# Kernel optimization log

Measured on AMD Instinct MI355X. Metric: run time of the kernel, lower is better.

The kernel has to match this reference:

```python
import jax, jax.numpy as jnp
import numpy as np
import math

H = 32          # num heads
D_NOPE = 128
D_ROPE = 64
D_QK = D_NOPE + D_ROPE   # 192
D_V = 128
KV_LORA = 512
EPS = 1e-6
ROPE_THETA = 10000.0
FACTOR = 40.0
BETA_FAST, BETA_SLOW = 32.0, 1.0
ORIG_MAX_POS = 4096
MSCALE_ALL_DIM = 1.0


def _yarn_inv_freq():
    dim = D_ROPE
    pos_freqs = ROPE_THETA ** (np.arange(0, dim, 2, dtype=np.float64) / dim)
    inv_extra = 1.0 / pos_freqs
    inv_inter = 1.0 / (FACTOR * pos_freqs)

    def corr_dim(n_rot):
        return dim * math.log(ORIG_MAX_POS / (n_rot * 2 * math.pi)) / (2 * math.log(ROPE_THETA))
    low = max(math.floor(corr_dim(BETA_FAST)), 0)
    high = min(math.ceil(corr_dim(BETA_SLOW)), dim - 1)
    ramp = np.clip((np.arange(dim // 2, dtype=np.float64) - low) / max(high - low, 1e-3), 0, 1)
    inv_freq_mask = 1.0 - ramp  # extrapolation_factor = 1
    inv_freq = inv_inter * (1 - inv_freq_mask) + inv_extra * inv_freq_mask
    return jnp.asarray(inv_freq, dtype=jnp.float32)  # [D_ROPE//2]


def _apply_rope_gptj(x, cos, sin):
    # x: [T, n, D_ROPE]; cos/sin: [T, D_ROPE//2]; interleaved (is_neox_style=False)
    x2 = x.reshape(*x.shape[:-1], D_ROPE // 2, 2)
    x1, xo = x2[..., 0], x2[..., 1]
    c = cos[:, None, :]
    s = sin[:, None, :]
    r1 = x1 * c - xo * s
    r2 = xo * c + x1 * s
    return jnp.stack([r1, r2], axis=-1).reshape(x.shape)


def _rmsnorm(x, w):
    var = jnp.mean(x.astype(jnp.float32) ** 2, axis=-1, keepdims=True)
    return (x * jax.lax.rsqrt(var + EPS)) * w


def setup_inputs() -> dict:
    key = jax.random.key(0)
    ks = jax.random.split(key, 8)
    T, HID = 2048, 4096
    def w(k, shape, fan_in):
        return jax.random.normal(k, shape, dtype=jnp.float32) * (1.0 / math.sqrt(fan_in))
    return {
        "positions": jnp.arange(T, dtype=jnp.int32),
        "hidden_states": jax.random.normal(ks[0], (T, HID), dtype=jnp.float32),
        "Wqa": w(ks[1], (HID, 1536), HID),
        "q_a_ln": jnp.ones((1536,), dtype=jnp.float32),
        "Wqb": w(ks[2], (1536, H * D_QK), 1536),
        "Wkva": w(ks[3], (HID, KV_LORA + D_ROPE), HID),
        "kv_a_ln": jnp.ones((KV_LORA,), dtype=jnp.float32),
        "Wkvb": w(ks[4], (KV_LORA, H * (D_NOPE + D_V)), KV_LORA),
        "Wo": w(ks[5], (H * D_V, HID), H * D_V),
    }


def reference(positions, hidden_states, Wqa, q_a_ln, Wqb, Wkva, kv_a_ln, Wkvb, Wo):
    T = hidden_states.shape[0]
    # softmax scaling with yarn mscale correction
    mscale = 0.1 * MSCALE_ALL_DIM * math.log(FACTOR) + 1.0
    scaling = (D_QK ** -0.5) * mscale * mscale

    # --- low-rank Q path ---
    q = hidden_states @ Wqa                       # [T, 1536]
    q = _rmsnorm(q, q_a_ln)
    q = (q @ Wqb).reshape(T, H, D_QK)             # [T, H, 192]
    q_nope, q_pe = q[..., :D_NOPE], q[..., D_NOPE:]

    # --- low-rank latent KV path ---
    latent = hidden_states @ Wkva                 # [T, 576]
    kv_a = _rmsnorm(latent[:, :KV_LORA], kv_a_ln) # [T, 512]
    k_pe = latent[:, None, KV_LORA:]              # [T, 1, 64]
    kv = (kv_a @ Wkvb).reshape(T, H, D_NOPE + D_V)
    k_nope = kv[..., :D_NOPE]                     # [T, H, 128]
    v = kv[..., D_NOPE:]                          # [T, H, 128]

    # --- decoupled RoPE on rope slice only ---
    inv_freq = _yarn_inv_freq()
    freqs = positions.astype(jnp.float32)[:, None] * inv_freq[None, :]  # [T, 32]
    cos, sin = jnp.cos(freqs), jnp.sin(freqs)
    q_pe = _apply_rope_gptj(q_pe, cos, sin)       # [T, H, 64]
    k_pe = _apply_rope_gptj(k_pe, cos, sin)       # [T, 1, 64]

    q = jnp.concatenate([q_nope, q_pe], axis=-1)                      # [T, H, 192]
    k = jnp.concatenate([k_nope, jnp.broadcast_to(k_pe, (T, H, D_ROPE))], axis=-1)

    # --- causal MHA over assembled K/V ---
    scores = jnp.einsum('thd,shd->hts', q, k) * scaling               # [H, T, T]
    causal = positions[None, :, None] >= positions[None, None, :]
    scores = jnp.where(causal, scores, jnp.finfo(scores.dtype).min)
    probs = jax.nn.softmax(scores, axis=-1)
    attn = jnp.einsum('hts,shd->thd', probs, v).reshape(T, H * D_V)
    return attn @ Wo                                                   # [T, 4096]
```

## Files before the change

kernel.cpp:

```cpp
#include <hip/hip_runtime.h>
#include <math.h>

typedef __bf16 bf16x8 __attribute__((ext_vector_type(8)));
typedef float f32x4 __attribute__((ext_vector_type(4)));
typedef unsigned short u16;
typedef unsigned int u32;

#define T_SEQ 2048
#define NHEAD 32

__device__ __forceinline__ u16 f2bu(float f){
  u32 u = __float_as_uint(f);
  u32 r = (u + 0x7fffu + ((u >> 16) & 1u)) >> 16;
  return (u16)r;
}

__device__ __forceinline__ void gload_lds16(const void* g, void* l){
  __builtin_amdgcn_global_load_lds((const __attribute__((address_space(1))) u32*)g,
                                   (__attribute__((address_space(3))) u32*)l, 16, 0, 0);
}

__global__ void cast_f32_bf16(const float* __restrict__ in, u16* __restrict__ out, int n4){
  int i = blockIdx.x * blockDim.x + threadIdx.x;
  int stride = gridDim.x * blockDim.x;
  for (; i < n4; i += stride){
    float4 v = ((const float4*)in)[i];
    ushort4 o;
    o.x = f2bu(v.x); o.y = f2bu(v.y); o.z = f2bu(v.z); o.w = f2bu(v.w);
    ((ushort4*)out)[i] = o;
  }
}

__device__ __forceinline__ void tc_body(const float* __restrict__ src, u16* __restrict__ dst,
                                        int K, int N, int k0, int n0){
  __shared__ float tile[64][65];
  int t = threadIdx.x;
  int rr = t >> 4, c4 = (t & 15) * 4;
  #pragma unroll
  for (int i = 0; i < 4; i++){
    int r = rr + i * 16;
    int n = n0 + c4;
    float4 v;
    if (n < N) v = *(const float4*)(src + (size_t)(k0 + r) * N + n);
    else       v = make_float4(0.f, 0.f, 0.f, 0.f);
    tile[r][c4]     = v.x;
    tile[r][c4 + 1] = v.y;
    tile[r][c4 + 2] = v.z;
    tile[r][c4 + 3] = v.w;
  }
  __syncthreads();
  #pragma unroll
  for (int i = 0; i < 4; i++){
    int n = rr + i * 16;
    ushort4 o;
    o.x = f2bu(tile[c4 + 0][n]);
    o.y = f2bu(tile[c4 + 1][n]);
    o.z = f2bu(tile[c4 + 2][n]);
    o.w = f2bu(tile[c4 + 3][n]);
    *(ushort4*)(dst + (size_t)(n0 + n) * K + k0 + c4) = o;
  }
}

__global__ __launch_bounds__(256) void transpose_batch(
    const float* __restrict__ Wqa, u16* __restrict__ WqaT,
    const float* __restrict__ Wkva, u16* __restrict__ WkvaT,
    const float* __restrict__ Wqb, u16* __restrict__ WqbT,
    const float* __restrict__ Wkvb, u16* __restrict__ WkvbT,
    const float* __restrict__ Wo, u16* __restrict__ WoT){
  int bid = blockIdx.x;
  const float* s; u16* d; int K, N, gx, l;
  if (bid < 1536)      { s = Wqa;  d = WqaT;  K = 4096; N = 1536; gx = 64; l = bid; }
  else if (bid < 2176) { s = Wkva; d = WkvaT; K = 4096; N = 576;  gx = 64; l = bid - 1536; }
  else if (bid < 4480) { s = Wqb;  d = WqbT;  K = 1536; N = 6144; gx = 24; l = bid - 2176; }
  else if (bid < 5504) { s = Wkvb; d = WkvbT; K = 512;  N = 8192; gx = 8;  l = bid - 4480; }
  else                 { s = Wo;   d = WoT;   K = 4096; N = 4096; gx = 64; l = bid - 5504; }
  tc_body(s, d, K, N, (l % gx) * 64, (l / gx) * 64);
}

__global__ void rope_table(const int* __restrict__ positions, float* __restrict__ cosT,
                           float* __restrict__ sinT, float lo, float denom){
  int idx = blockIdx.x * blockDim.x + threadIdx.x;
  if (idx >= T_SEQ * 32) return;
  int t = idx >> 5, i = idx & 31;
  float pf = powf(10000.f, (float)i / 32.f);
  float inv_extra = 1.f / pf;
  float inv_inter = 1.f / (40.f * pf);
  float ramp = fminf(fmaxf(((float)i - lo) / denom, 0.f), 1.f);
  float invf = inv_inter * ramp + inv_extra * (1.f - ramp);
  float fr = (float)positions[t] * invf;
  cosT[idx] = cosf(fr);
  sinT[idx] = sinf(fr);
}

__global__ void rmsnorm_cast(const float* __restrict__ in, int istride, int n,
                             const float* __restrict__ w, u16* __restrict__ out, int ostride){
  int row = blockIdx.x;
  const float* x = in + (size_t)row * istride;
  float ss = 0.f;
  for (int c = threadIdx.x; c < n; c += blockDim.x){ float v = x[c]; ss += v * v; }
  #pragma unroll
  for (int off = 1; off < 64; off <<= 1) ss += __shfl_xor(ss, off);
  __shared__ float wsum[4];
  if ((threadIdx.x & 63) == 0) wsum[threadIdx.x >> 6] = ss;
  __syncthreads();
  float tot = wsum[0] + wsum[1] + wsum[2] + wsum[3];
  float scale = rsqrtf(tot / (float)n + 1e-6f);
  for (int c = threadIdx.x; c < n; c += blockDim.x)
    out[(size_t)row * ostride + c] = f2bu(x[c] * scale * w[c]);
}

__global__ void rope_kpe(const float* __restrict__ lat, int lstride, int loff,
                         const float* __restrict__ cosT,
                         const float* __restrict__ sinT, u16* __restrict__ kpe){
  int idx = blockIdx.x * blockDim.x + threadIdx.x;
  if (idx >= T_SEQ * 32) return;
  int t = idx >> 5, i = idx & 31;
  float x1 = lat[(size_t)t * lstride + loff + 2 * i];
  float x2 = lat[(size_t)t * lstride + loff + 2 * i + 1];
  float c = cosT[idx], s = sinT[idx];
  kpe[t * 64 + 2 * i]     = f2bu(x1 * c - x2 * s);
  kpe[t * 64 + 2 * i + 1] = f2bu(x2 * c + x1 * s);
}

__global__ void build_vt(const u16* __restrict__ Vtmp, u16* __restrict__ Vt){
  __shared__ u16 tile[128][72];
  int t0 = blockIdx.x * 64;
  int h = blockIdx.y;
  #pragma unroll
  for (int i = 0; i < 32; i++){
    int lin = threadIdx.x + i * 256;
    int tt = lin >> 7, dd = lin & 127;
    tile[dd][tt] = Vtmp[(size_t)(t0 + tt) * 4096 + h * 128 + dd];
  }
  __syncthreads();
  #pragma unroll
  for (int i = 0; i < 32; i++){
    int lin = threadIdx.x + i * 256;
    int dd = lin >> 6, tt = lin & 63;
    Vt[(size_t)(h * 128 + dd) * T_SEQ + t0 + tt] = tile[dd][tt];
  }
}

template<int EPI>
__global__ __launch_bounds__(256) void gemm_bt(const u16* __restrict__ A, const u16* __restrict__ BT,
                                               float* __restrict__ C, u16* __restrict__ O1,
                                               u16* __restrict__ O2,
                                               const float* __restrict__ cosT,
                                               const float* __restrict__ sinT,
                                               float scaling, int M, int N, int K){
  __shared__ __align__(1024) char lds[32768];
  const int tid = threadIdx.x;
  const int wave = tid >> 6, lane = tid & 63;
  const int lg = lane >> 4, lm = lane & 15;

  int gx = gridDim.x;
  int nwg = gx * gridDim.y;
  int orig = blockIdx.y * gx + blockIdx.x;
  int qq = nwg >> 3, rr_ = nwg & 7, xc = orig & 7, rest = orig >> 3;
  int wg = (xc < rr_ ? xc * (qq + 1) : rr_ * (qq + 1) + (xc - rr_) * qq) + rest;
  const int bn = (wg % gx) * 128, bm = (wg / gx) * 128;

  const int wr = (wave >> 1) * 64, wc = (wave & 1) * 64;
  f32x4 acc[4][4] = {};
  int srow[2], scol[2], soff[2];
  #pragma unroll
  for (int j = 0; j < 2; j++){
    int o = (wave * 2 + j) * 1024 + lane * 16;
    int row = o >> 6;
    int cg = ((o >> 4) & 3) ^ ((row >> 1) & 3);
    srow[j] = row; scol[j] = cg * 8; soff[j] = (wave * 2 + j) * 1024;
  }

  #pragma unroll
  for (int j = 0; j < 2; j++){
    gload_lds16(A  + (size_t)(bm + srow[j]) * K + scol[j], lds + soff[j]);
    gload_lds16(BT + (size_t)(bn + srow[j]) * K + scol[j], lds + 16384 + soff[j]);
  }

  int cur = 0;
  for (int k0 = 0; k0 < K; k0 += 32){
    if (k0 + 32 < K){
      char* dA = lds + (cur ^ 1) * 8192;
      char* dB = lds + 16384 + (cur ^ 1) * 8192;
      #pragma unroll
      for (int j = 0; j < 2; j++){
        gload_lds16(A  + (size_t)(bm + srow[j]) * K + k0 + 32 + scol[j], dA + soff[j]);
        gload_lds16(BT + (size_t)(bn + srow[j]) * K + k0 + 32 + scol[j], dB + soff[j]);
      }
      asm volatile("s_waitcnt vmcnt(4)" ::: "memory");
    } else {
      asm volatile("s_waitcnt vmcnt(0)" ::: "memory");
    }
    __builtin_amdgcn_sched_barrier(0);
    __builtin_amdgcn_s_barrier();

    const char* ldsA = lds + cur * 8192;
    const char* ldsB = lds + 16384 + cur * 8192;
    bf16x8 af[4], bfr[4];
    #pragma unroll
    for (int m = 0; m < 4; m++){
      int r = wr + m * 16 + lm;
      af[m] = *(const bf16x8*)(ldsA + r * 64 + ((lg ^ ((r >> 1) & 3)) << 4));
    }
    #pragma unroll
    for (int n = 0; n < 4; n++){
      int r = wc + n * 16 + lm;
      bfr[n] = *(const bf16x8*)(ldsB + r * 64 + ((lg ^ ((r >> 1) & 3)) << 4));
    }
    __builtin_amdgcn_s_setprio(1);
    #pragma unroll
    for (int m = 0; m < 4; m++)
      #pragma unroll
      for (int n = 0; n < 4; n++)
        acc[m][n] = __builtin_amdgcn_mfma_f32_16x16x32_bf16(af[m], bfr[n], acc[m][n], 0, 0, 0);
    __builtin_amdgcn_s_setprio(0);
    __builtin_amdgcn_s_barrier();
    cur ^= 1;
  }

  #pragma unroll
  for (int m = 0; m < 4; m++)
    #pragma unroll
    for (int n = 0; n < 4; n++)
      #pragma unroll
      for (int q = 0; q < 4; q++){
        int r = bm + wr + m * 16 + lg * 4 + q;
        int c = bn + wc + n * 16 + lm;
        float v = acc[m][n][q];
        if (EPI == 0){
          C[(size_t)r * N + c] = v;
        } else if (EPI == 1){
          float vp = __shfl_xor(v, 1);
          int h = c / 192, d = c - h * 192;
          float outv;
          if (d < 128) outv = v;
          else {
            int i = (d - 128) >> 1;
            float co = cosT[r * 32 + i], si = sinT[r * 32 + i];
            outv = (d & 1) ? (v * co + vp * si) : (v * co - vp * si);
          }
          O1[(size_t)h * T_SEQ * 192 + (size_t)r * 192 + d] = f2bu(outv * scaling);
        } else {
          int h = c >> 8, d = c & 255;
          if (d < 128) O1[(size_t)h * T_SEQ * 128 + (size_t)r * 128 + d] = f2bu(v);
          else         O2[(size_t)r * 4096 + h * 128 + (d - 128)] = f2bu(v);
        }
      }
}

__global__ __launch_bounds__(512, 4) void flash_attn(const u16* __restrict__ Qp, const u16* __restrict__ Kp,
                                                     const u16* __restrict__ kpe, const u16* __restrict__ Vt,
                                                     u16* __restrict__ attnb){
  const int b = blockIdx.x;
  const int h = (b & 7) + 8 * ((b >> 3) & 3);
  const int qt = 15 - (b >> 5);
  const int tid = threadIdx.x;
  const int wave = tid >> 6, lane = tid & 63;
  const int lg = lane >> 4, lm = lane & 15;
  const int qbase = qt * 128 + wave * 16;

  __shared__ __align__(1024) char lds[51200];
  u16* Pw = (u16*)(lds + 40960 + wave * 1280);

  const u16* KpH = Kp + (size_t)h * T_SEQ * 128;
  const u16* VtH = Vt + (size_t)h * 128 * T_SEQ;

  int kO[2], kLoc[2], kPE[2];
  #pragma unroll
  for (int j = 0; j < 2; j++){
    int o = tid + 512 * j;
    int r = (o / 24) & 31, c = o % 24;
    int cx = c ^ (r & 7);
    kO[j] = o * 16;
    if (cx < 16){ kPE[j] = 0; kLoc[j] = r * 128 + cx * 8; }
    else        { kPE[j] = 1; kLoc[j] = r * 64 + (cx - 16) * 8; }
  }
  int vO, vSrc;
  { int o = tid; int d = o >> 2, c = o & 3; vO = o * 16; vSrc = d * T_SEQ + ((c ^ ((d >> 1) & 3)) << 3); }

  #define STAGE_KV(t, bi)                                                              \
    do {                                                                               \
      char* _k = lds + (bi) * 12288;                                                   \
      char* _v = lds + 24576 + (bi) * 8192;                                            \
      { const u16* _s = kPE[0] ? (kpe + (size_t)(t) * 2048 + kLoc[0])                  \
                               : (KpH + (size_t)(t) * 4096 + kLoc[0]);                 \
        gload_lds16(_s, _k + kO[0]); }                                                 \
      if (tid < 256){                                                                  \
        const u16* _s = kPE[1] ? (kpe + (size_t)(t) * 2048 + kLoc[1])                  \
                               : (KpH + (size_t)(t) * 4096 + kLoc[1]);                 \
        gload_lds16(_s, _k + kO[1]); }                                                 \
      gload_lds16(VtH + vSrc + (t) * 32, _v + vO);                                     \
    } while (0)

  const int nt = 4 * qt + 4;

  bf16x8 qf[6];
  const u16* Qbase = Qp + (size_t)(h * T_SEQ + qbase + lm) * 192 + lg * 8;
  #pragma unroll
  for (int dk = 0; dk < 6; dk++) qf[dk] = *(const bf16x8*)(Qbase + dk * 32);

  f32x4 o_[8] = {};
  float m_[4], l_[4];
  #pragma unroll
  for (int q = 0; q < 4; q++){ m_[q] = -3.0e38f; l_[q] = 0.f; }

  STAGE_KV(0, 0);

  #pragma unroll 1
  for (int kt = 0; kt < nt; kt++){
    const int t0 = kt * 32;
    const int bsel = kt & 1;
    asm volatile("s_waitcnt vmcnt(0)" ::: "memory");
    __builtin_amdgcn_sched_barrier(0);
    __builtin_amdgcn_s_barrier();
    if (kt + 1 < nt) STAGE_KV(kt + 1, bsel ^ 1);
    const char* Kb = lds + bsel * 12288;
    const char* Vb = lds + 24576 + bsel * 8192;

    f32x4 s_[2] = {};
    __builtin_amdgcn_s_setprio(1);
    #pragma unroll
    for (int hh = 0; hh < 2; hh++){
      const int r = hh * 16 + lm;
      const int rb = r * 384, rx = r & 7;
      #pragma unroll
      for (int dk = 0; dk < 6; dk++){
        bf16x8 kf = *(const bf16x8*)(Kb + rb + (((dk * 4 + lg) ^ rx) << 4));
        s_[hh] = __builtin_amdgcn_mfma_f32_16x16x32_bf16(qf[dk], kf, s_[hh], 0, 0, 0);
      }
    }
    __builtin_amdgcn_s_setprio(0);
    #pragma unroll
    for (int hh = 0; hh < 2; hh++)
      #pragma unroll
      for (int q = 0; q < 4; q++){
        int col = t0 + hh * 16 + lm;
        int qrow = qbase + lg * 4 + q;
        if (col > qrow) s_[hh][q] = -3.0e38f;
      }
    float pm[4];
    #pragma unroll
    for (int q = 0; q < 4; q++) pm[q] = fmaxf(s_[0][q], s_[1][q]);
    int ok = (pm[0] <= m_[0] + 8.f) & (pm[1] <= m_[1] + 8.f) &
             (pm[2] <= m_[2] + 8.f) & (pm[3] <= m_[3] + 8.f);
    if (!__all(ok)){
      #pragma unroll
      for (int q = 0; q < 4; q++){
        float v = pm[q];
        #pragma unroll
        for (int off = 8; off; off >>= 1) v = fmaxf(v, __shfl_xor(v, off));
        float mn = fmaxf(m_[q], v);
        float alpha = (m_[q] <= -1.0e37f) ? 0.f : exp2f(m_[q] - mn);
        l_[q] *= alpha;
        #pragma unroll
        for (int n = 0; n < 8; n++) o_[n][q] *= alpha;
        m_[q] = mn;
      }
    }
    #pragma unroll
    for (int q = 0; q < 4; q++){
      #pragma unroll
      for (int hh = 0; hh < 2; hh++){
        float p = exp2f(s_[hh][q] - m_[q]);
        l_[q] += p;
        Pw[(lg * 4 + q) * 40 + hh * 16 + lm] = f2bu(p);
      }
    }
    asm volatile("s_waitcnt lgkmcnt(0)" ::: "memory");
    __builtin_amdgcn_sched_barrier(0);
    bf16x8 pf = *(const bf16x8*)((const char*)Pw + lm * 80 + lg * 16);
    __builtin_amdgcn_s_setprio(1);
    #pragma unroll
    for (int n = 0; n < 8; n++){
      const int d = n * 16 + lm;
      bf16x8 vf = *(const bf16x8*)(Vb + d * 64 + ((lg ^ ((d >> 1) & 3)) << 4));
      o_[n] = __builtin_amdgcn_mfma_f32_16x16x32_bf16(pf, vf, o_[n], 0, 0, 0);
    }
    __builtin_amdgcn_s_setprio(0);
  }

  #pragma unroll
  for (int q = 0; q < 4; q++){
    #pragma unroll
    for (int off = 8; off; off >>= 1) l_[q] += __shfl_xor(l_[q], off);
  }
  float inv[4];
  #pragma unroll
  for (int q = 0; q < 4; q++) inv[q] = 1.f / l_[q];
  #pragma unroll
  for (int n = 0; n < 8; n++)
    #pragma unroll
    for (int q = 0; q < 4; q++){
      int r = qbase + lg * 4 + q;
      attnb[(size_t)r * 4096 + h * 128 + n * 16 + lm] = f2bu(o_[n][q] * inv[q]);
    }
  #undef STAGE_KV
}

extern "C" void kernel_launch(void* const* d_in, const int* in_sizes, int n_in,
                              void* d_out, int out_size, void* d_ws, size_t ws_size,
                              hipStream_t stream){
  const int*   positions = (const int*)d_in[0];
  const float* hidden    = (const float*)d_in[1];
  const float* Wqa       = (const float*)d_in[2];
  const float* q_a_ln    = (const float*)d_in[3];
  const float* Wqb       = (const float*)d_in[4];
  const float* Wkva      = (const float*)d_in[5];
  const float* kv_a_ln   = (const float*)d_in[6];
  const float* Wkvb      = (const float*)d_in[7];
  const float* Wo        = (const float*)d_in[8];
  float* out = (float*)d_out;
  char* ws = (char*)d_ws;

  const size_t o_hidB  = 0;
  const size_t o_cos   = 16777216;
  const size_t o_sin   = 17039360;
  const size_t o_kpe   = 17301504;
  const size_t o_comb  = 17563648;
  const size_t o_qln   = 35389440;
  const size_t o_kva   = 41680896;
  const size_t o_WqaT  = 43778048;
  const size_t o_WkvaT = 56360960;
  const size_t o_WqbT  = 61603840;
  const size_t o_WkvbT = 80478208;
  const size_t o_Qp    = 88866816;
  const size_t o_Kp    = 114032640;
  const size_t o_Vtmp  = 130809856;
  const size_t o_Vt    = 147587072;
  const size_t o_WoT   = 164364288;

  u16*   hidB  = (u16*)(ws + o_hidB);
  u16*   attnb = (u16*)(ws + o_hidB);
  float* cosT  = (float*)(ws + o_cos);
  float* sinT  = (float*)(ws + o_sin);
  u16*   kpe   = (u16*)(ws + o_kpe);
  float* comb  = (float*)(ws + o_comb);
  u16*   qln   = (u16*)(ws + o_qln);
  u16*   kva   = (u16*)(ws + o_kva);
  u16*   WqaT  = (u16*)(ws + o_WqaT);
  u16*   WkvaT = (u16*)(ws + o_WkvaT);
  u16*   WqbT  = (u16*)(ws + o_WqbT);
  u16*   WkvbT = (u16*)(ws + o_WkvbT);
  u16*   Qp    = (u16*)(ws + o_Qp);
  u16*   Kp    = (u16*)(ws + o_Kp);
  u16*   Vtmp  = (u16*)(ws + o_Vtmp);
  u16*   Vt    = (u16*)(ws + o_Vt);
  u16*   WoT   = (u16*)(ws + o_WoT);

  double mscale = 0.1 * log(40.0) + 1.0;
  double scaling_d = pow(192.0, -0.5) * mscale * mscale;
  float scaling_log2 = (float)(scaling_d * 1.4426950408889634);
  const double PI = 3.14159265358979323846;
  double cd_fast = 64.0 * log(4096.0 / (32.0 * 2.0 * PI)) / (2.0 * log(10000.0));
  double cd_slow = 64.0 * log(4096.0 / ( 1.0 * 2.0 * PI)) / (2.0 * log(10000.0));
  double lo_d = fmax(floor(cd_fast), 0.0);
  double hi_d = fmin(ceil(cd_slow), 63.0);
  float lo = (float)lo_d;
  float denom = (float)fmax(hi_d - lo_d, 0.001);

  transpose_batch<<<9600, 256, 0, stream>>>(Wqa, WqaT, Wkva, WkvaT, Wqb, WqbT,
                                            Wkvb, WkvbT, Wo, WoT);
  cast_f32_bf16<<<2048, 256, 0, stream>>>(hidden, hidB, T_SEQ * 4096 / 4);
  rope_table<<<256, 256, 0, stream>>>(positions, cosT, sinT, lo, denom);
  gemm_bt<0><<<dim3(2176 / 128, 2048 / 128), 256, 0, stream>>>(hidB, WqaT, comb, nullptr, nullptr,
                                                               nullptr, nullptr, 0.f, 2048, 2176, 4096);
  rmsnorm_cast<<<2048, 256, 0, stream>>>(comb, 2176, 1536, q_a_ln, qln, 1536);
  rmsnorm_cast<<<2048, 256, 0, stream>>>(comb + 1536, 2176, 512, kv_a_ln, kva, 512);
  rope_kpe<<<256, 256, 0, stream>>>(comb, 2176, 2048, cosT, sinT, kpe);
  gemm_bt<1><<<dim3(6144 / 128, 2048 / 128), 256, 0, stream>>>(qln, WqbT, nullptr, Qp, nullptr,
                                                               cosT, sinT, scaling_log2, 2048, 6144, 1536);
  gemm_bt<2><<<dim3(8192 / 128, 2048 / 128), 256, 0, stream>>>(kva, WkvbT, nullptr, Kp, Vtmp,
                                                               nullptr, nullptr, 0.f, 2048, 8192, 512);
  build_vt<<<dim3(T_SEQ / 64, NHEAD), 256, 0, stream>>>(Vtmp, Vt);
  flash_attn<<<512, 512, 0, stream>>>(Qp, Kp, kpe, Vt, attnb);
  gemm_bt<0><<<dim3(4096 / 128, 2048 / 128), 256, 0, stream>>>(attnb, WoT, out, nullptr, nullptr,
                                                               nullptr, nullptr, 0.f, 2048, 4096, 4096);
}
```

Measured before the change: 416.4 us.

## Fuse V transpose into KV-b GEMM epilogue and rebalance attention tile order

The KV up-projection GEMM epilogue now writes V directly in transposed [head*128+d][T] layout using 4-element vector stores, so the separate build_vt kernel and its intermediate buffer go away. This saves one launch plus a full read and write of V. The flash attention block-to-query-tile mapping also changes: the first half of the blocks runs heavy tiles first and the second half runs light tiles first, meant to balance the causal workload across waves of blocks. The transposed stores are strided by T_SEQ across lanes and may coalesce less well.

```diff
diff --git a/kernel.cpp b/kernel.cpp
--- a/kernel.cpp
+++ b/kernel.cpp
@@ -122,25 +122,6 @@
   kpe[t * 64 + 2 * i + 1] = f2bu(x2 * c + x1 * s);
 }
 
-__global__ void build_vt(const u16* __restrict__ Vtmp, u16* __restrict__ Vt){
-  __shared__ u16 tile[128][72];
-  int t0 = blockIdx.x * 64;
-  int h = blockIdx.y;
-  #pragma unroll
-  for (int i = 0; i < 32; i++){
-    int lin = threadIdx.x + i * 256;
-    int tt = lin >> 7, dd = lin & 127;
-    tile[dd][tt] = Vtmp[(size_t)(t0 + tt) * 4096 + h * 128 + dd];
-  }
-  __syncthreads();
-  #pragma unroll
-  for (int i = 0; i < 32; i++){
-    int lin = threadIdx.x + i * 256;
-    int dd = lin >> 6, tt = lin & 63;
-    Vt[(size_t)(h * 128 + dd) * T_SEQ + t0 + tt] = tile[dd][tt];
-  }
-}
-
 template<int EPI>
 __global__ __launch_bounds__(256) void gemm_bt(const u16* __restrict__ A, const u16* __restrict__ BT,
                                                float* __restrict__ C, u16* __restrict__ O1,
@@ -221,31 +202,42 @@
   #pragma unroll
   for (int m = 0; m < 4; m++)
     #pragma unroll
-    for (int n = 0; n < 4; n++)
-      #pragma unroll
-      for (int q = 0; q < 4; q++){
-        int r = bm + wr + m * 16 + lg * 4 + q;
-        int c = bn + wc + n * 16 + lm;
-        float v = acc[m][n][q];
-        if (EPI == 0){
-          C[(size_t)r * N + c] = v;
-        } else if (EPI == 1){
+    for (int n = 0; n < 4; n++){
+      const int r0 = bm + wr + m * 16 + lg * 4;
+      const int c  = bn + wc + n * 16 + lm;
+      if (EPI == 0){
+        #pragma unroll
+        for (int q = 0; q < 4; q++)
+          C[(size_t)(r0 + q) * N + c] = acc[m][n][q];
+      } else if (EPI == 1){
+        #pragma unroll
+        for (int q = 0; q < 4; q++){
+          float v = acc[m][n][q];
           float vp = __shfl_xor(v, 1);
           int h = c / 192, d = c - h * 192;
           float outv;
           if (d < 128) outv = v;
           else {
             int i = (d - 128) >> 1;
-            float co = cosT[r * 32 + i], si = sinT[r * 32 + i];
+            float co = cosT[(r0 + q) * 32 + i], si = sinT[(r0 + q) * 32 + i];
             outv = (d & 1) ? (v * co + vp * si) : (v * co - vp * si);
           }
-          O1[(size_t)h * T_SEQ * 192 + (size_t)r * 192 + d] = f2bu(outv * scaling);
+          O1[(size_t)h * T_SEQ * 192 + (size_t)(r0 + q) * 192 + d] = f2bu(outv * scaling);
+        }
+      } else {
+        int h = c >> 8, d = c & 255;
+        if (d < 128){
+          #pragma unroll
+          for (int q = 0; q < 4; q++)
+            O1[(size_t)h * T_SEQ * 128 + (size_t)(r0 + q) * 128 + d] = f2bu(acc[m][n][q]);
         } else {
-          int h = c >> 8, d = c & 255;
-          if (d < 128) O1[(size_t)h * T_SEQ * 128 + (size_t)r * 128 + d] = f2bu(v);
-          else         O2[(size_t)r * 4096 + h * 128 + (d - 128)] = f2bu(v);
+          ushort4 o;
+          o.x = f2bu(acc[m][n][0]); o.y = f2bu(acc[m][n][1]);
+          o.z = f2bu(acc[m][n][2]); o.w = f2bu(acc[m][n][3]);
+          *(ushort4*)(O2 + (size_t)(h * 128 + (d - 128)) * T_SEQ + r0) = o;
         }
       }
+    }
 }
 
 __global__ __launch_bounds__(512, 4) void flash_attn(const u16* __restrict__ Qp, const u16* __restrict__ Kp,
@@ -253,7 +245,7 @@
                                                      u16* __restrict__ attnb){
   const int b = blockIdx.x;
   const int h = (b & 7) + 8 * ((b >> 3) & 3);
-  const int qt = 15 - (b >> 5);
+  const int qt = (b < 256) ? (15 - (b >> 5)) : ((b - 256) >> 5);
   const int tid = threadIdx.x;
   const int wave = tid >> 6, lane = tid & 63;
   const int lg = lane >> 4, lm = lane & 15;
@@ -425,7 +417,6 @@
   const size_t o_WkvbT = 80478208;
   const size_t o_Qp    = 88866816;
   const size_t o_Kp    = 114032640;
-  const size_t o_Vtmp  = 130809856;
   const size_t o_Vt    = 147587072;
   const size_t o_WoT   = 164364288;
 
@@ -443,7 +434,6 @@
   u16*   WkvbT = (u16*)(ws + o_WkvbT);
   u16*   Qp    = (u16*)(ws + o_Qp);
   u16*   Kp    = (u16*)(ws + o_Kp);
-  u16*   Vtmp  = (u16*)(ws + o_Vtmp);
   u16*   Vt    = (u16*)(ws + o_Vt);
   u16*   WoT   = (u16*)(ws + o_WoT);
 
@@ -469,9 +459,8 @@
   rope_kpe<<<256, 256, 0, stream>>>(comb, 2176, 2048, cosT, sinT, kpe);
   gemm_bt<1><<<dim3(6144 / 128, 2048 / 128), 256, 0, stream>>>(qln, WqbT, nullptr, Qp, nullptr,
                                                                cosT, sinT, scaling_log2, 2048, 6144, 1536);
-  gemm_bt<2><<<dim3(8192 / 128, 2048 / 128), 256, 0, stream>>>(kva, WkvbT, nullptr, Kp, Vtmp,
+  gemm_bt<2><<<dim3(8192 / 128, 2048 / 128), 256, 0, stream>>>(kva, WkvbT, nullptr, Kp, Vt,
                                                                nullptr, nullptr, 0.f, 2048, 8192, 512);
-  build_vt<<<dim3(T_SEQ / 64, NHEAD), 256, 0, stream>>>(Vtmp, Vt);
   flash_attn<<<512, 512, 0, stream>>>(Qp, Kp, kpe, Vt, attnb);
   gemm_bt<0><<<dim3(4096 / 128, 2048 / 128), 256, 0, stream>>>(attnb, WoT, out, nullptr, nullptr,
                                                                nullptr, nullptr, 0.f, 2048, 4096, 4096);
```

After: 397.4 us. 4.6% less time.
